# Optimization experiments

Measured on AMD Instinct MI355X. Metric: run time of the kernel, lower is better.

Reference implementation:

```python
import jax, jax.numpy as jnp
import numpy as np

N_PTS = 131072
IN_CH = 63
IN_CH_VIEWS = 27
WIDTH = 256
NUM_HEADS = 4
SCALE = 0.05


def setup_inputs() -> dict:
    key = jax.random.key(0)
    ks = jax.random.split(key, 12)
    H, W = NUM_HEADS, WIDTH
    inp = {
        'x': jax.random.normal(ks[0], (N_PTS, IN_CH + IN_CH_VIEWS), jnp.float32),
        'head_idx': jax.random.randint(ks[1], (N_PTS,), 0, NUM_HEADS),
        # shared trunk: layer0 63->256, layers1..3 256->256 (no skip before split_at=4)
        'W0': jax.random.normal(ks[2], (IN_CH, W), jnp.float32) * SCALE,
        'b0': jnp.zeros((W,), jnp.float32),
        'Ws': jax.random.normal(ks[3], (3, W, W), jnp.float32) * SCALE,
        'bs': jnp.zeros((3, W), jnp.float32),
        # per-head tails: g=4 in skips -> (W+63)->W, then g=5..7 W->W
        'tW0': jax.random.normal(ks[4], (H, W + IN_CH, W), jnp.float32) * SCALE,
        'tb0': jnp.zeros((H, W), jnp.float32),
        'tWs': jax.random.normal(ks[5], (H, 3, W, W), jnp.float32) * SCALE,
        'tbs': jnp.zeros((H, 3, W), jnp.float32),
        # per-head viewdirs output heads
        'featW': jax.random.normal(ks[6], (H, W, W), jnp.float32) * SCALE,
        'featb': jnp.zeros((H, W), jnp.float32),
        'alphaW': jax.random.normal(ks[7], (H, W, 1), jnp.float32) * SCALE,
        'alphab': jnp.zeros((H, 1), jnp.float32),
        'viewsW': jax.random.normal(ks[8], (H, IN_CH_VIEWS + W, W // 2), jnp.float32) * SCALE,
        'viewsb': jnp.zeros((H, W // 2), jnp.float32),
        'rgbW': jax.random.normal(ks[9], (H, W // 2, 3), jnp.float32) * SCALE,
        'rgbb': jnp.zeros((H, 3), jnp.float32),
    }
    return inp


def reference(x, head_idx, W0, b0, Ws, bs, tW0, tb0, tWs, tbs,
              featW, featb, alphaW, alphab, viewsW, viewsb, rgbW, rgbb):
    input_pts = x[:, :IN_CH]          # [N, 63]
    input_views = x[:, IN_CH:]        # [N, 27]

    # shared trunk (layers 0..3, no skip hits in this range)
    h = jax.nn.relu(input_pts @ W0 + b0)
    for i in range(Ws.shape[0]):
        h = jax.nn.relu(h @ Ws[i] + bs[i])

    # per-head tails, computed densely for ALL heads (as in the original)
    # first tail layer g=4 is a skip layer: concat input_pts
    ht = jnp.concatenate([input_pts, h], axis=-1)          # [N, 319]
    ha = jax.nn.relu(jnp.einsum('nf,hfo->nho', ht, tW0) + tb0[None])  # [N, H, 256]
    for j in range(tWs.shape[1]):
        ha = jax.nn.relu(jnp.einsum('nho,hop->nhp', ha, tWs[:, j]) + tbs[None, :, j])

    # per-head viewdir output heads
    alpha = jnp.einsum('nho,hop->nhp', ha, alphaW) + alphab[None]     # [N, H, 1]
    feat = jnp.einsum('nho,hop->nhp', ha, featW) + featb[None]        # [N, H, 256]
    views_b = jnp.broadcast_to(input_views[:, None, :], (x.shape[0], feat.shape[1], IN_CH_VIEWS))
    hv = jnp.concatenate([feat, views_b], axis=-1)                    # [N, H, 283]
    hv = jax.nn.relu(jnp.einsum('nho,hop->nhp', hv, viewsW) + viewsb[None])
    rgb = jnp.einsum('nho,hop->nhp', hv, rgbW) + rgbb[None]           # [N, H, 3]

    outs = jnp.concatenate([rgb, alpha], axis=-1)                     # [N, H, 4]
    sel = jnp.take_along_axis(outs, head_idx[:, None, None], axis=1)[:, 0]  # [N, 4]
    return sel
```

## Files before the change

kernel.cpp:

```cpp
#include <hip/hip_runtime.h>

#define N_PTS 131072
#define TILE 64
#define THREADS 512
#define REGION 40960

typedef __bf16 bf16;
typedef __bf16 bf16x8 __attribute__((ext_vector_type(8)));
typedef float f32x4 __attribute__((ext_vector_type(4)));

#define WS_PERM_OFF   256
#define WS_WPACK_OFF  (256 + 4 * REGION * 4)
#define OFF_W0     0
#define OFF_WS     16384
#define OFF_TW0    212992
#define OFF_TWS    540672
#define OFF_FEATW  1327104
#define OFF_VIEWSW 1589248
#define TOTAL_PACK 1736704

#define PTS_BASE 0
#define H_BASE   8192
#define B_BASE   40960
#define LDS_BYTES 73728

__device__ __forceinline__ unsigned swz(unsigned base, unsigned row, unsigned rowstride,
                                        unsigned kbyte) {
  return (base + row * rowstride + kbyte) ^ ((row & 7u) << 4);
}

__device__ __forceinline__ void gload_lds16(const bf16* g, char* l) {
  __builtin_amdgcn_global_load_lds(
      (const __attribute__((address_space(1))) void*)g,
      (__attribute__((address_space(3))) void*)l, 16, 0, 0);
}

__global__ void k_pack(const float* __restrict__ W0, const float* __restrict__ Ws,
                       const float* __restrict__ tW0, const float* __restrict__ tWs,
                       const float* __restrict__ featW, const float* __restrict__ viewsW,
                       bf16* __restrict__ out, const int* __restrict__ head,
                       int* __restrict__ ctrl, int* __restrict__ perm) {
  int gid = blockIdx.x * blockDim.x + threadIdx.x;
  if (gid < N_PTS) {
    int h = head[gid];
    int lane = threadIdx.x & 63;
    #pragma unroll
    for (int hh = 0; hh < 4; ++hh) {
      unsigned long long m = __ballot(h == hh);
      if (m == 0ull) continue;
      int leader = __builtin_ctzll(m);
      int base = 0;
      if (lane == leader) base = atomicAdd(&ctrl[16 + hh], __popcll(m));
      base = __shfl(base, leader);
      if (h == hh) {
        int rank = __popcll(m & ((1ull << lane) - 1ull));
        perm[hh * REGION + base + rank] = gid;
      }
    }
  }

  for (int idx = gid; idx < TOTAL_PACK; idx += gridDim.x * blockDim.x) {
    float v;
    if (idx < OFF_WS) {
      int o = idx >> 6, k = idx & 63;
      v = (k < 63) ? W0[k * 256 + o] : 0.f;
    } else if (idx < OFF_TW0) {
      int i = idx - OFF_WS; int l = i >> 16, r = i & 65535, o = r >> 8, k = r & 255;
      v = Ws[l * 65536 + k * 256 + o];
    } else if (idx < OFF_TWS) {
      int i = idx - OFF_TW0; int h = i / 81920, r = i % 81920, o = r / 320, k = r % 320;
      v = (k < 63) ? tW0[(h * 319 + k) * 256 + o]
                   : (k == 63 ? 0.f : tW0[(h * 319 + k - 1) * 256 + o]);
    } else if (idx < OFF_FEATW) {
      int i = idx - OFF_TWS; int hj = i >> 16, r = i & 65535, o = r >> 8, k = r & 255;
      v = tWs[(hj * 256 + k) * 256 + o];
    } else if (idx < OFF_VIEWSW) {
      int i = idx - OFF_FEATW; int h = i >> 16, r = i & 65535, o = r >> 8, k = r & 255;
      v = featW[(h * 256 + k) * 256 + o];
    } else {
      int i = idx - OFF_VIEWSW; int h = i / 36864, r = i % 36864, o = r / 288, k = r % 288;
      v = (k < 283) ? viewsW[(h * 283 + k) * 128 + o] : 0.f;
    }
    out[idx] = (bf16)v;
  }
}

template <int MR, int NF, bool RELU, int A0KC, int A1KC, int OUTS>
__device__ __forceinline__ void mfma_layer(char* lds, const bf16* __restrict__ Wt, int wK,
                                           const float* __restrict__ bias,
                                           int a0_base, int a0_stride,
                                           int a1_base, int a1_stride,
                                           int out_base, int out_stride,
                                           int lane, int wave) {
  const int l15 = lane & 15, l4 = lane >> 4;
  const int wr = wave >> 2, wc = wave & 3;
  constexpr int KC = A0KC + A1KC;
  constexpr int ISSUES = OUTS / 128;
  f32x4 acc[MR][NF];
  #pragma unroll
  for (int m = 0; m < MR; ++m)
    #pragma unroll
    for (int n = 0; n < NF; ++n) acc[m][n] = (f32x4){0.f, 0.f, 0.f, 0.f};

  const int r0 = wr * (MR * 16);
  const int c0 = wc * (NF * 16);

  const char* bbase[NF];
  #pragma unroll
  for (int n = 0; n < NF; ++n) {
    int col = c0 + n * 16 + l15;
    bbase[n] = lds + B_BASE + col * 64 + ((l4 ^ ((col >> 1) & 3)) << 4);
  }

  unsigned a_cur[MR], a_xor[MR];
  #pragma unroll
  for (int m = 0; m < MR; ++m) {
    int row = r0 + m * 16 + l15;
    a_cur[m] = a0_base + row * a0_stride + l4 * 16;
    a_xor[m] = (row & 7u) << 4;
  }

  const bf16* gsrc[ISSUES];
  #pragma unroll
  for (int s = 0; s < ISSUES; ++s) {
    int reg = wave * ISSUES + s;
    int o = reg * 16 + (lane >> 2);
    int j = lane & 3;
    gsrc[s] = Wt + o * wK + ((j ^ ((o >> 1) & 3)) << 3);
  }

  #pragma unroll
  for (int s = 0; s < ISSUES; ++s) {
    gload_lds16(gsrc[s], lds + B_BASE + (wave * ISSUES + s) * 1024);
    gsrc[s] += 32;
  }

  auto dostep = [&](int kc, int bufoff) {
    asm volatile("s_waitcnt vmcnt(0)" ::: "memory");
    __builtin_amdgcn_s_barrier();

    if (kc + 1 < KC) {
      #pragma unroll
      for (int s = 0; s < ISSUES; ++s) {
        gload_lds16(gsrc[s], lds + B_BASE + (bufoff ^ 16384) + (wave * ISSUES + s) * 1024);
        gsrc[s] += 32;
      }
    }
    if (A1KC > 0 && kc == A0KC) {
      #pragma unroll
      for (int m = 0; m < MR; ++m)
        a_cur[m] = a1_base + (r0 + m * 16 + l15) * a1_stride + l4 * 16;
    }

    bf16x8 a[MR], b[NF];
    #pragma unroll
    for (int m = 0; m < MR; ++m) {
      a[m] = *(const bf16x8*)(lds + (a_cur[m] ^ a_xor[m]));
      a_cur[m] += 64;
    }
    #pragma unroll
    for (int n = 0; n < NF; ++n)
      b[n] = *(const bf16x8*)(bbase[n] + bufoff);

    __builtin_amdgcn_s_setprio(1);
    #pragma unroll
    for (int n = 0; n < NF; ++n)
      #pragma unroll
      for (int m = 0; m < MR; ++m)
        acc[m][n] = __builtin_amdgcn_mfma_f32_16x16x32_bf16(a[m], b[n], acc[m][n], 0, 0, 0);
    __builtin_amdgcn_s_setprio(0);
  };

  #pragma unroll 1
  for (int kc = 0; kc + 1 < KC; kc += 2) {
    dostep(kc, 0);
    dostep(kc + 1, 16384);
  }
  if (KC & 1) dostep(KC - 1, 0);

  __builtin_amdgcn_s_barrier();

  #pragma unroll
  for (int n = 0; n < NF; ++n) {
    int col = c0 + n * 16 + l15;
    float bv = bias[col];
    #pragma unroll
    for (int m = 0; m < MR; ++m) {
      #pragma unroll
      for (int j = 0; j < 4; ++j) {
        float v = acc[m][n][j] + bv;
        if (RELU) v = fmaxf(v, 0.f);
        int row = r0 + m * 16 + l4 * 4 + j;
        *(bf16*)(lds + swz(out_base, row, out_stride, col * 2)) = (bf16)v;
      }
    }
  }
  __syncthreads();
}

__global__ __launch_bounds__(THREADS, 4) void k_main(
    const float* __restrict__ x, const int* __restrict__ ctrl, const int* __restrict__ perm,
    const bf16* __restrict__ wpack,
    const float* __restrict__ b0, const float* __restrict__ bs,
    const float* __restrict__ tb0p, const float* __restrict__ tbsp,
    const float* __restrict__ featb, const float* __restrict__ alphaW,
    const float* __restrict__ alphab, const float* __restrict__ viewsb,
    const float* __restrict__ rgbW, const float* __restrict__ rgbb,
    float* __restrict__ outp) {
  __shared__ __attribute__((aligned(16))) char lds[LDS_BYTES];
  __shared__ int pidx[TILE];
  __shared__ float alpha_s[TILE];

  const int tid = threadIdx.x;
  const int lane = tid & 63, wave = tid >> 6;

  const int hh = blockIdx.x / (REGION / TILE);
  const int start = (blockIdx.x % (REGION / TILE)) * TILE;
  const int cnt = ctrl[16 + hh];
  if (start >= cnt) return;
  const int nv = min(TILE, cnt - start);

  if (tid < TILE) pidx[tid] = (tid < nv) ? perm[hh * REGION + start + tid] : -1;
  __syncthreads();

  for (int i = tid; i < TILE * 64; i += THREADS) {
    int row = i >> 6, c = i & 63;
    int p = pidx[row];
    float v = (p >= 0 && c < 63) ? x[p * 90 + c] : 0.f;
    *(bf16*)(lds + swz(PTS_BASE, row, 128, c * 2)) = (bf16)v;
  }
  __syncthreads();

  const bf16* W0p    = wpack + OFF_W0;
  const bf16* Wsp    = wpack + OFF_WS;
  const bf16* tW0p   = wpack + OFF_TW0 + hh * 81920;
  const bf16* tWsp   = wpack + OFF_TWS + hh * 3 * 65536;
  const bf16* featWp = wpack + OFF_FEATW + hh * 65536;
  const bf16* viewsWp= wpack + OFF_VIEWSW + hh * 36864;

  mfma_layer<2, 4, true, 2, 0, 256>(lds, W0p, 64, b0, PTS_BASE, 128, 0, 0, H_BASE, 512, lane, wave);
  mfma_layer<2, 4, true, 8, 0, 256>(lds, Wsp,          256, bs,       H_BASE, 512, 0, 0, H_BASE, 512, lane, wave);
  mfma_layer<2, 4, true, 8, 0, 256>(lds, Wsp + 65536,  256, bs + 256, H_BASE, 512, 0, 0, H_BASE, 512, lane, wave);
  mfma_layer<2, 4, true, 8, 0, 256>(lds, Wsp + 131072, 256, bs + 512, H_BASE, 512, 0, 0, H_BASE, 512, lane, wave);
  mfma_layer<2, 4, true, 2, 8, 256>(lds, tW0p, 320, tb0p + hh * 256,
                                    PTS_BASE, 128, H_BASE, 512, H_BASE, 512, lane, wave);

  for (int i = tid; i < TILE * 32; i += THREADS) {
    int row = i >> 5, c = i & 31;
    int p = pidx[row];
    float v = (p >= 0 && c < 27) ? x[p * 90 + 63 + c] : 0.f;
    *(bf16*)(lds + swz(PTS_BASE, row, 128, c * 2)) = (bf16)v;
  }
  __syncthreads();

  mfma_layer<2, 4, true, 8, 0, 256>(lds, tWsp,          256, tbsp + hh * 768,       H_BASE, 512, 0, 0, H_BASE, 512, lane, wave);
  mfma_layer<2, 4, true, 8, 0, 256>(lds, tWsp + 65536,  256, tbsp + hh * 768 + 256, H_BASE, 512, 0, 0, H_BASE, 512, lane, wave);
  mfma_layer<2, 4, true, 8, 0, 256>(lds, tWsp + 131072, 256, tbsp + hh * 768 + 512, H_BASE, 512, 0, 0, H_BASE, 512, lane, wave);

  if (wave < 4) {
    int p = wave * 16 + (lane & 15);
    int kq = lane >> 4;
    const float* aW = alphaW + hh * 256;
    float s = 0.f;
    for (int i = 0; i < 8; ++i) {
      int k = kq * 64 + i * 8;
      bf16x8 hv8 = *(const bf16x8*)(lds + swz(H_BASE, p, 512, k * 2));
      #pragma unroll
      for (int j = 0; j < 8; ++j) s += (float)hv8[j] * aW[k + j];
    }
    s += __shfl_xor(s, 16);
    s += __shfl_xor(s, 32);
    if (kq == 0) alpha_s[p] = s + alphab[hh];
  }

  mfma_layer<2, 4, false, 8, 0, 256>(lds, featWp, 256, featb + hh * 256,
                                     H_BASE, 512, 0, 0, H_BASE, 512, lane, wave);
  mfma_layer<2, 2, true, 8, 1, 128>(lds, viewsWp, 288, viewsb + hh * 128,
                                    H_BASE, 512, PTS_BASE, 128, H_BASE, 512, lane, wave);

  if (wave < 4) {
    int p = wave * 16 + (lane & 15);
    int kq = lane >> 4;
    const float* rW = rgbW + hh * 128 * 3;
    float r0 = 0.f, r1 = 0.f, r2 = 0.f;
    for (int i = 0; i < 4; ++i) {
      int k = kq * 32 + i * 8;
      bf16x8 hv8 = *(const bf16x8*)(lds + swz(H_BASE, p, 512, k * 2));
      #pragma unroll
      for (int j = 0; j < 8; ++j) {
        float hvf = (float)hv8[j];
        r0 += hvf * rW[(k + j) * 3 + 0];
        r1 += hvf * rW[(k + j) * 3 + 1];
        r2 += hvf * rW[(k + j) * 3 + 2];
      }
    }
    r0 += __shfl_xor(r0, 16); r0 += __shfl_xor(r0, 32);
    r1 += __shfl_xor(r1, 16); r1 += __shfl_xor(r1, 32);
    r2 += __shfl_xor(r2, 16); r2 += __shfl_xor(r2, 32);
    if (kq == 0 && p < nv) {
      int pt = pidx[p];
      float4 o = make_float4(r0 + rgbb[hh * 3 + 0], r1 + rgbb[hh * 3 + 1],
                             r2 + rgbb[hh * 3 + 2], alpha_s[p]);
      *(float4*)(outp + pt * 4) = o;
    }
  }
}

extern "C" void kernel_launch(void* const* d_in, const int* in_sizes, int n_in,
                              void* d_out, int out_size, void* d_ws, size_t ws_size,
                              hipStream_t stream) {
  const float* x      = (const float*)d_in[0];
  const int*   head   = (const int*)d_in[1];
  const float* W0     = (const float*)d_in[2];
  const float* b0     = (const float*)d_in[3];
  const float* Ws     = (const float*)d_in[4];
  const float* bs     = (const float*)d_in[5];
  const float* tW0    = (const float*)d_in[6];
  const float* tb0    = (const float*)d_in[7];
  const float* tWs    = (const float*)d_in[8];
  const float* tbs    = (const float*)d_in[9];
  const float* featW  = (const float*)d_in[10];
  const float* featb  = (const float*)d_in[11];
  const float* alphaW = (const float*)d_in[12];
  const float* alphab = (const float*)d_in[13];
  const float* viewsW = (const float*)d_in[14];
  const float* viewsb = (const float*)d_in[15];
  const float* rgbW   = (const float*)d_in[16];
  const float* rgbb   = (const float*)d_in[17];

  int*  ctrl  = (int*)d_ws;
  int*  perm  = (int*)((char*)d_ws + WS_PERM_OFF);
  bf16* wpack = (bf16*)((char*)d_ws + WS_WPACK_OFF);

  hipMemsetAsync(ctrl, 0, 256, stream);
  k_pack<<<2048, 256, 0, stream>>>(W0, Ws, tW0, tWs, featW, viewsW, wpack, head, ctrl, perm);
  k_main<<<4 * (REGION / TILE), THREADS, 0, stream>>>(x, ctrl, perm, wpack,
                                                      b0, bs, tb0, tbs, featb, alphaW, alphab,
                                                      viewsb, rgbW, rgbb, (float*)d_out);
}
```

Baseline: 396.3 us.

## Triple-buffer weight staging and keep point/view inputs in registers

```diff
diff --git a/kernel.cpp b/kernel.cpp
--- a/kernel.cpp
+++ b/kernel.cpp
@@ -19,10 +19,9 @@
 #define OFF_VIEWSW 1589248
 #define TOTAL_PACK 1736704
 
-#define PTS_BASE 0
-#define H_BASE   8192
-#define B_BASE   40960
-#define LDS_BYTES 73728
+#define H_BASE 0
+#define B_BASE 32768
+#define LDS_BYTES 81920
 
 __device__ __forceinline__ unsigned swz(unsigned base, unsigned row, unsigned rowstride,
                                         unsigned kbyte) {
@@ -33,6 +32,13 @@
   __builtin_amdgcn_global_load_lds(
       (const __attribute__((address_space(1))) void*)g,
       (__attribute__((address_space(3))) void*)l, 16, 0, 0);
+}
+
+template <int N>
+__device__ __forceinline__ void wait_stage() {
+  if constexpr (N == 0)      asm volatile("s_waitcnt vmcnt(0)" ::: "memory");
+  else if constexpr (N == 1) asm volatile("s_waitcnt vmcnt(1)" ::: "memory");
+  else                       asm volatile("s_waitcnt vmcnt(2)" ::: "memory");
 }
 
 __global__ void k_pack(const float* __restrict__ W0, const float* __restrict__ Ws,
@@ -60,41 +66,88 @@
   }
 
   for (int idx = gid; idx < TOTAL_PACK; idx += gridDim.x * blockDim.x) {
-    float v;
-    if (idx < OFF_WS) {
-      int o = idx >> 6, k = idx & 63;
+    float v; int dst;
+    if (idx < 16384) {
+      int k = idx >> 8, o = idx & 255;
       v = (k < 63) ? W0[k * 256 + o] : 0.f;
-    } else if (idx < OFF_TW0) {
-      int i = idx - OFF_WS; int l = i >> 16, r = i & 65535, o = r >> 8, k = r & 255;
-      v = Ws[l * 65536 + k * 256 + o];
-    } else if (idx < OFF_TWS) {
-      int i = idx - OFF_TW0; int h = i / 81920, r = i % 81920, o = r / 320, k = r % 320;
+      dst = OFF_W0 + o * 64 + k;
+    } else if (idx < 212992) {
+      int i = idx - 16384; int l = i >> 16, r = i & 65535, k = r >> 8, o = r & 255;
+      v = Ws[i];
+      dst = OFF_WS + l * 65536 + o * 256 + k;
+    } else if (idx < 540672) {
+      int i = idx - 212992; int h = i / 81920, r = i % 81920, k = r >> 8, o = r & 255;
       v = (k < 63) ? tW0[(h * 319 + k) * 256 + o]
                    : (k == 63 ? 0.f : tW0[(h * 319 + k - 1) * 256 + o]);
-    } else if (idx < OFF_FEATW) {
-      int i = idx - OFF_TWS; int hj = i >> 16, r = i & 65535, o = r >> 8, k = r & 255;
-      v = tWs[(hj * 256 + k) * 256 + o];
-    } else if (idx < OFF_VIEWSW) {
-      int i = idx - OFF_FEATW; int h = i >> 16, r = i & 65535, o = r >> 8, k = r & 255;
-      v = featW[(h * 256 + k) * 256 + o];
+      dst = OFF_TW0 + h * 81920 + o * 320 + k;
+    } else if (idx < 1327104) {
+      int i = idx - 540672; int hj = i >> 16, r = i & 65535, k = r >> 8, o = r & 255;
+      v = tWs[i];
+      dst = OFF_TWS + hj * 65536 + o * 256 + k;
+    } else if (idx < 1589248) {
+      int i = idx - 1327104; int h = i >> 16, r = i & 65535, k = r >> 8, o = r & 255;
+      v = featW[i];
+      dst = OFF_FEATW + h * 65536 + o * 256 + k;
     } else {
-      int i = idx - OFF_VIEWSW; int h = i / 36864, r = i % 36864, o = r / 288, k = r % 288;
+      int i = idx - 1589248; int h = i / 36864, r = i % 36864, k = r >> 7, o = r & 127;
       v = (k < 283) ? viewsW[(h * 283 + k) * 128 + o] : 0.f;
-    }
-    out[idx] = (bf16)v;
-  }
-}
-
-template <int MR, int NF, bool RELU, int A0KC, int A1KC, int OUTS>
-__device__ __forceinline__ void mfma_layer(char* lds, const bf16* __restrict__ Wt, int wK,
-                                           const float* __restrict__ bias,
-                                           int a0_base, int a0_stride,
-                                           int a1_base, int a1_stride,
-                                           int out_base, int out_stride,
+      dst = OFF_VIEWSW + h * 36864 + o * 288 + k;
+    }
+    out[dst] = (bf16)v;
+  }
+}
+
+#define PIPE_STEP(WAITN, DO_STAGE, LOAD_A)                                     \
+  do {                                                                         \
+    wait_stage<WAITN>();                                                       \
+    __builtin_amdgcn_s_barrier();                                              \
+    if (DO_STAGE) {                                                            \
+      _Pragma("unroll")                                                        \
+      for (int s = 0; s < ISSUES; ++s) {                                       \
+        gload_lds16(gsrc[s], sbase + sd + s * 1024);                           \
+        gsrc[s] += 32;                                                         \
+      }                                                                        \
+      sd = (sd == 32768) ? 0 : sd + 16384;                                     \
+    }                                                                          \
+    bf16x8 a[MR];                                                              \
+    LOAD_A;                                                                    \
+    bf16x8 b[NF];                                                              \
+    {                                                                          \
+      const char* bp = lds + breg + sr;                                        \
+      _Pragma("unroll")                                                        \
+      for (int n = 0; n < NF; ++n) b[n] = *(const bf16x8*)(bp + n * 1024);     \
+    }                                                                          \
+    sr = (sr == 32768) ? 0 : sr + 16384;                                       \
+    __builtin_amdgcn_s_setprio(1);                                             \
+    _Pragma("unroll")                                                          \
+    for (int n = 0; n < NF; ++n)                                               \
+      _Pragma("unroll")                                                        \
+      for (int m = 0; m < MR; ++m)                                             \
+        acc[m][n] =                                                            \
+            __builtin_amdgcn_mfma_f32_16x16x32_bf16(a[m], b[n], acc[m][n],     \
+                                                    0, 0, 0);                  \
+    __builtin_amdgcn_s_setprio(0);                                             \
+  } while (0)
+
+#define LOADA_REG(K)                                                           \
+  { _Pragma("unroll") for (int m = 0; m < MR; ++m) a[m] = aregs[(K) * MR + m]; }
+
+#define LOADA_LDS                                                              \
+  {                                                                            \
+    unsigned va = acur ^ axor;                                                 \
+    _Pragma("unroll")                                                          \
+    for (int m = 0; m < MR; ++m) a[m] = *(const bf16x8*)(lds + va + m * 8192); \
+    acur += 64;                                                                \
+  }
+
+template <int MR, int NF, bool RELU, int RKC, int LKC, bool REG_FIRST, int OUTS>
+__device__ __forceinline__ void mfma_layer(char* lds, const bf16* __restrict__ Wt,
+                                           int wK, const float* __restrict__ bias,
+                                           const bf16x8* aregs,
                                            int lane, int wave) {
   const int l15 = lane & 15, l4 = lane >> 4;
   const int wr = wave >> 2, wc = wave & 3;
-  constexpr int KC = A0KC + A1KC;
+  constexpr int KC = RKC + LKC;
   constexpr int ISSUES = OUTS / 128;
   f32x4 acc[MR][NF];
   #pragma unroll
@@ -105,20 +158,10 @@
   const int r0 = wr * (MR * 16);
   const int c0 = wc * (NF * 16);
 
-  const char* bbase[NF];
-  #pragma unroll
-  for (int n = 0; n < NF; ++n) {
-    int col = c0 + n * 16 + l15;
-    bbase[n] = lds + B_BASE + col * 64 + ((l4 ^ ((col >> 1) & 3)) << 4);
-  }
-
-  unsigned a_cur[MR], a_xor[MR];
-  #pragma unroll
-  for (int m = 0; m < MR; ++m) {
-    int row = r0 + m * 16 + l15;
-    a_cur[m] = a0_base + row * a0_stride + l4 * 16;
-    a_xor[m] = (row & 7u) << 4;
-  }
+  const int breg = B_BASE + (c0 + l15) * 64 + ((l4 ^ ((l15 >> 1) & 3)) << 4);
+
+  unsigned acur = (unsigned)((r0 + l15) * 512 + l4 * 16);
+  const unsigned axor = (l15 & 7u) << 4;
 
   const bf16* gsrc[ISSUES];
   #pragma unroll
@@ -128,55 +171,40 @@
     int j = lane & 3;
     gsrc[s] = Wt + o * wK + ((j ^ ((o >> 1) & 3)) << 3);
   }
-
-  #pragma unroll
-  for (int s = 0; s < ISSUES; ++s) {
-    gload_lds16(gsrc[s], lds + B_BASE + (wave * ISSUES + s) * 1024);
-    gsrc[s] += 32;
-  }
-
-  auto dostep = [&](int kc, int bufoff) {
-    asm volatile("s_waitcnt vmcnt(0)" ::: "memory");
-    __builtin_amdgcn_s_barrier();
-
-    if (kc + 1 < KC) {
-      #pragma unroll
-      for (int s = 0; s < ISSUES; ++s) {
-        gload_lds16(gsrc[s], lds + B_BASE + (bufoff ^ 16384) + (wave * ISSUES + s) * 1024);
-        gsrc[s] += 32;
-      }
-    }
-    if (A1KC > 0 && kc == A0KC) {
-      #pragma unroll
-      for (int m = 0; m < MR; ++m)
-        a_cur[m] = a1_base + (r0 + m * 16 + l15) * a1_stride + l4 * 16;
-    }
-
-    bf16x8 a[MR], b[NF];
-    #pragma unroll
-    for (int m = 0; m < MR; ++m) {
-      a[m] = *(const bf16x8*)(lds + (a_cur[m] ^ a_xor[m]));
-      a_cur[m] += 64;
-    }
-    #pragma unroll
-    for (int n = 0; n < NF; ++n)
-      b[n] = *(const bf16x8*)(bbase[n] + bufoff);
-
-    __builtin_amdgcn_s_setprio(1);
-    #pragma unroll
-    for (int n = 0; n < NF; ++n)
-      #pragma unroll
-      for (int m = 0; m < MR; ++m)
-        acc[m][n] = __builtin_amdgcn_mfma_f32_16x16x32_bf16(a[m], b[n], acc[m][n], 0, 0, 0);
-    __builtin_amdgcn_s_setprio(0);
-  };
-
-  #pragma unroll 1
-  for (int kc = 0; kc + 1 < KC; kc += 2) {
-    dostep(kc, 0);
-    dostep(kc + 1, 16384);
-  }
-  if (KC & 1) dostep(KC - 1, 0);
+  char* sbase = lds + B_BASE + (wave * ISSUES) * 1024;
+
+  #pragma unroll
+  for (int s = 0; s < ISSUES; ++s) { gload_lds16(gsrc[s], sbase + s * 1024); gsrc[s] += 32; }
+  #pragma unroll
+  for (int s = 0; s < ISSUES; ++s) { gload_lds16(gsrc[s], sbase + 16384 + s * 1024); gsrc[s] += 32; }
+
+  int sr = 0;
+  int sd = 32768;
+
+  if constexpr (REG_FIRST && RKC >= 1) {
+    if constexpr (KC == 1) PIPE_STEP(0, false, LOADA_REG(0));
+    else                   PIPE_STEP(ISSUES, (2 < KC), LOADA_REG(0));
+  }
+  if constexpr (REG_FIRST && RKC >= 2) {
+    if constexpr (KC == 2) PIPE_STEP(0, false, LOADA_REG(1));
+    else                   PIPE_STEP(ISSUES, (3 < KC), LOADA_REG(1));
+  }
+
+  if constexpr (LKC > 0) {
+    constexpr int kc0 = REG_FIRST ? RKC : 0;
+    constexpr bool last_in_lds = (REG_FIRST || RKC == 0);
+    constexpr int kcend = REG_FIRST ? KC : LKC;
+    constexpr int loop_end = kcend - (last_in_lds ? 1 : 0);
+    #pragma unroll 1
+    for (int kc = kc0; kc < loop_end; ++kc) {
+      PIPE_STEP(ISSUES, (kc + 2 < KC), LOADA_LDS);
+    }
+    if constexpr (last_in_lds) PIPE_STEP(0, false, LOADA_LDS);
+  }
+
+  if constexpr (!REG_FIRST && RKC >= 1) {
+    PIPE_STEP(0, false, LOADA_REG(0));
+  }
 
   __builtin_amdgcn_s_barrier();
 
@@ -191,7 +219,7 @@
         float v = acc[m][n][j] + bv;
         if (RELU) v = fmaxf(v, 0.f);
         int row = r0 + m * 16 + l4 * 4 + j;
-        *(bf16*)(lds + swz(out_base, row, out_stride, col * 2)) = (bf16)v;
+        *(bf16*)(lds + swz(H_BASE, row, 512, col * 2)) = (bf16)v;
       }
     }
   }
@@ -208,28 +236,51 @@
     const float* __restrict__ rgbW, const float* __restrict__ rgbb,
     float* __restrict__ outp) {
   __shared__ __attribute__((aligned(16))) char lds[LDS_BYTES];
-  __shared__ int pidx[TILE];
-  __shared__ float alpha_s[TILE];
 
   const int tid = threadIdx.x;
   const int lane = tid & 63, wave = tid >> 6;
+  const int l15 = lane & 15, l4 = lane >> 4;
 
   const int hh = blockIdx.x / (REGION / TILE);
   const int start = (blockIdx.x % (REGION / TILE)) * TILE;
   const int cnt = ctrl[16 + hh];
   if (start >= cnt) return;
   const int nv = min(TILE, cnt - start);
-
-  if (tid < TILE) pidx[tid] = (tid < nv) ? perm[hh * REGION + start + tid] : -1;
-  __syncthreads();
-
-  for (int i = tid; i < TILE * 64; i += THREADS) {
-    int row = i >> 6, c = i & 63;
-    int p = pidx[row];
-    float v = (p >= 0 && c < 63) ? x[p * 90 + c] : 0.f;
-    *(bf16*)(lds + swz(PTS_BASE, row, 128, c * 2)) = (bf16)v;
-  }
-  __syncthreads();
+  const int permbase = hh * REGION + start;
+
+  bf16x8 ptsreg[4];
+  bf16x8 viewsreg[2];
+  {
+    const int wr = wave >> 2;
+    #pragma unroll
+    for (int m = 0; m < 2; ++m) {
+      int row = wr * 32 + m * 16 + l15;
+      bool valid = (start + row) < cnt;
+      int p = valid ? perm[permbase + row] : 0;
+      const float* xr = x + p * 90;
+      #pragma unroll
+      for (int rkc = 0; rkc < 2; ++rkc) {
+        int k0 = rkc * 32 + l4 * 8;
+        bf16x8 f;
+        #pragma unroll
+        for (int j = 0; j < 8; ++j) {
+          int k = k0 + j;
+          f[j] = (bf16)((valid && k < 63) ? xr[k] : 0.f);
+        }
+        ptsreg[rkc * 2 + m] = f;
+      }
+      {
+        int k0 = l4 * 8;
+        bf16x8 f;
+        #pragma unroll
+        for (int j = 0; j < 8; ++j) {
+          int k = k0 + j;
+          f[j] = (bf16)((valid && k < 27) ? xr[63 + k] : 0.f);
+        }
+        viewsreg[m] = f;
+      }
+    }
+  }
 
   const bf16* W0p    = wpack + OFF_W0;
   const bf16* Wsp    = wpack + OFF_WS;
@@ -238,48 +289,43 @@
   const bf16* featWp = wpack + OFF_FEATW + hh * 65536;
   const bf16* viewsWp= wpack + OFF_VIEWSW + hh * 36864;
 
-  mfma_layer<2, 4, true, 2, 0, 256>(lds, W0p, 64, b0, PTS_BASE, 128, 0, 0, H_BASE, 512, lane, wave);
-  mfma_layer<2, 4, true, 8, 0, 256>(lds, Wsp,          256, bs,       H_BASE, 512, 0, 0, H_BASE, 512, lane, wave);
-  mfma_layer<2, 4, true, 8, 0, 256>(lds, Wsp + 65536,  256, bs + 256, H_BASE, 512, 0, 0, H_BASE, 512, lane, wave);
-  mfma_layer<2, 4, true, 8, 0, 256>(lds, Wsp + 131072, 256, bs + 512, H_BASE, 512, 0, 0, H_BASE, 512, lane, wave);
-  mfma_layer<2, 4, true, 2, 8, 256>(lds, tW0p, 320, tb0p + hh * 256,
-                                    PTS_BASE, 128, H_BASE, 512, H_BASE, 512, lane, wave);
-
-  for (int i = tid; i < TILE * 32; i += THREADS) {
-    int row = i >> 5, c = i & 31;
-    int p = pidx[row];
-    float v = (p >= 0 && c < 27) ? x[p * 90 + 63 + c] : 0.f;
-    *(bf16*)(lds + swz(PTS_BASE, row, 128, c * 2)) = (bf16)v;
-  }
-  __syncthreads();
-
-  mfma_layer<2, 4, true, 8, 0, 256>(lds, tWsp,          256, tbsp + hh * 768,       H_BASE, 512, 0, 0, H_BASE, 512, lane, wave);
-  mfma_layer<2, 4, true, 8, 0, 256>(lds, tWsp + 65536,  256, tbsp + hh * 768 + 256, H_BASE, 512, 0, 0, H_BASE, 512, lane, wave);
-  mfma_layer<2, 4, true, 8, 0, 256>(lds, tWsp + 131072, 256, tbsp + hh * 768 + 512, H_BASE, 512, 0, 0, H_BASE, 512, lane, wave);
-
+  mfma_layer<2, 4, true, 2, 0, true,  256>(lds, W0p, 64, b0, ptsreg, lane, wave);
+  mfma_layer<2, 4, true, 0, 8, false, 256>(lds, Wsp,          256, bs,       nullptr, lane, wave);
+  mfma_layer<2, 4, true, 0, 8, false, 256>(lds, Wsp + 65536,  256, bs + 256, nullptr, lane, wave);
+  mfma_layer<2, 4, true, 0, 8, false, 256>(lds, Wsp + 131072, 256, bs + 512, nullptr, lane, wave);
+  mfma_layer<2, 4, true, 2, 8, true,  256>(lds, tW0p, 320, tb0p + hh * 256, ptsreg, lane, wave);
+
+  mfma_layer<2, 4, true, 0, 8, false, 256>(lds, tWsp,          256, tbsp + hh * 768,       nullptr, lane, wave);
+  mfma_layer<2, 4, true, 0, 8, false, 256>(lds, tWsp + 65536,  256, tbsp + hh * 768 + 256, nullptr, lane, wave);
+  mfma_layer<2, 4, true, 0, 8, false, 256>(lds, tWsp + 131072, 256, tbsp + hh * 768 + 512, nullptr, lane, wave);
+
+  float my_alpha = 0.f;
   if (wave < 4) {
-    int p = wave * 16 + (lane & 15);
-    int kq = lane >> 4;
+    int p = wave * 16 + l15;
+    int kq = l4 >> 1;
     const float* aW = alphaW + hh * 256;
     float s = 0.f;
-    for (int i = 0; i < 8; ++i) {
-      int k = kq * 64 + i * 8;
-      bf16x8 hv8 = *(const bf16x8*)(lds + swz(H_BASE, p, 512, k * 2));
-      #pragma unroll
-      for (int j = 0; j < 8; ++j) s += (float)hv8[j] * aW[k + j];
+    int kqq = lane >> 4;
+    for (int i = 0; i < 4; ++i) {
+      int k = kqq * 64 + i * 16;
+      bf16x8 h0 = *(const bf16x8*)(lds + swz(H_BASE, p, 512, k * 2));
+      bf16x8 h1 = *(const bf16x8*)(lds + swz(H_BASE, p, 512, (k + 8) * 2));
+      #pragma unroll
+      for (int j = 0; j < 8; ++j) s += (float)h0[j] * aW[k + j];
+      #pragma unroll
+      for (int j = 0; j < 8; ++j) s += (float)h1[j] * aW[k + 8 + j];
     }
     s += __shfl_xor(s, 16);
     s += __shfl_xor(s, 32);
-    if (kq == 0) alpha_s[p] = s + alphab[hh];
-  }
-
-  mfma_layer<2, 4, false, 8, 0, 256>(lds, featWp, 256, featb + hh * 256,
-                                     H_BASE, 512, 0, 0, H_BASE, 512, lane, wave);
-  mfma_layer<2, 2, true, 8, 1, 128>(lds, viewsWp, 288, viewsb + hh * 128,
-                                    H_BASE, 512, PTS_BASE, 128, H_BASE, 512, lane, wave);
+    my_alpha = s + alphab[hh];
+    (void)kq;
+  }
+
+  mfma_layer<2, 4, false, 0, 8, false, 256>(lds, featWp, 256, featb + hh * 256, nullptr, lane, wave);
+  mfma_layer<2, 2, true, 1, 8, false, 128>(lds, viewsWp, 288, viewsb + hh * 128, viewsreg, lane, wave);
 
   if (wave < 4) {
-    int p = wave * 16 + (lane & 15);
+    int p = wave * 16 + l15;
     int kq = lane >> 4;
     const float* rW = rgbW + hh * 128 * 3;
     float r0 = 0.f, r1 = 0.f, r2 = 0.f;
@@ -298,9 +344,9 @@
     r1 += __shfl_xor(r1, 16); r1 += __shfl_xor(r1, 32);
     r2 += __shfl_xor(r2, 16); r2 += __shfl_xor(r2, 32);
     if (kq == 0 && p < nv) {
-      int pt = pidx[p];
+      int pt = perm[permbase + p];
       float4 o = make_float4(r0 + rgbb[hh * 3 + 0], r1 + rgbb[hh * 3 + 1],
-                             r2 + rgbb[hh * 3 + 2], alpha_s[p]);
+                             r2 + rgbb[hh * 3 + 2], my_alpha);
       *(float4*)(outp + pt * 4) = o;
     }
   }
```

Result: no change. 392.8 us (-0.9%).
